# Performance work log

Measured on AMD Instinct MI355X. Metric: run time of the kernel, lower is better.

Reference implementation:

```python
import math
import jax, jax.numpy as jnp
import numpy as np

B, N, E, H, U = 8, 1024, 256, 4, 6
HD = E // H // 2  # head_dim = embed_dim // num_heads // 2 = 32
DEPTH = 1
LAMBDA_INIT = 1.0 - math.exp(-1.0 / DEPTH)


def setup_inputs() -> dict:
    key = jax.random.key(0)
    ks = jax.random.split(key, 8)
    x = jax.random.normal(ks[0], (B, N, E), dtype=jnp.float32)
    u = jax.random.normal(ks[1], (B, U, N, N), dtype=jnp.float32)
    # bool mask, True = masked out; p=0.2 so no row is fully masked
    umask = jax.random.bernoulli(ks[2], 0.2, (B, N, N, 1))
    v_w = jax.random.normal(ks[3], (E, E), dtype=jnp.float32) * (E ** -0.5)
    out_w = jax.random.normal(ks[4], (E, E), dtype=jnp.float32) * (E ** -0.5)
    u_w = jax.random.normal(ks[5], (2 * H, U), dtype=jnp.float32) * (U ** -0.5)  # 1x1 conv weight
    u_b = jnp.zeros((2 * H,), dtype=jnp.float32)
    lambda_q1 = jax.random.normal(ks[6], (100,), dtype=jnp.float32) * 0.1
    lambda_k1 = jax.random.normal(ks[7], (100,), dtype=jnp.float32) * 0.1
    return {"x": x, "u": u, "umask": umask, "v_w": v_w, "out_w": out_w,
            "u_w": u_w, "u_b": u_b, "lambda_q1": lambda_q1, "lambda_k1": lambda_k1}


def reference(x, u, umask, v_w, out_w, u_w, u_b, lambda_q1, lambda_k1):
    b, n, e = x.shape
    # v projection -> [B, H, N, 2*HD]
    v = jnp.einsum('bne,fe->bnf', x, v_w)
    v = v.reshape(b, n, H, 2 * HD).transpose(0, 2, 1, 3)
    # 1x1 conv over channel dim: [B, U, N, N] -> [B, 2H, N, N]
    scores = jnp.einsum('bcij,oc->boij', u, u_w) + u_b[None, :, None, None]
    # masked_fill with umask.transpose(3,1): [B,N,N,1] -> [B,1,N,N]
    mask = jnp.transpose(umask, (0, 3, 2, 1))
    scores = jnp.where(mask, -jnp.inf, scores)
    attn = jax.nn.softmax(scores, axis=-1)
    # differential beta (scalar)
    lambda_1 = jnp.exp(jnp.sum(lambda_q1 * lambda_k1))
    beta = jax.nn.sigmoid(lambda_1 * LAMBDA_INIT)
    attn = attn.reshape(b, H, 2, n, n)
    attn_w = attn[:, :, 0] - beta * attn[:, :, 1]  # [B, H, N, N]
    out = jnp.einsum('bhij,bhjd->bhid', attn_w, v)  # [B, H, N, 2HD]
    out = out.transpose(0, 2, 1, 3).reshape(b, n, e)
    out = jnp.einsum('bne,fe->bnf', out, out_w)
    return (out, attn_w, beta)
```

## Files before the change

### kernel.cpp

```cpp
#include <hip/hip_runtime.h>

#define Bb 8
#define Nn 1024
#define Ee 256
#define Hh 4
#define Uu 6
#define CH 8
#define HD2 64

static constexpr size_t OUT_ATTN = (size_t)Bb * Nn * Ee;
static constexpr size_t OUT_BETA = OUT_ATTN + (size_t)Bb * Hh * Nn * Nn;

static constexpr size_t WS_W     = 64;
static constexpr size_t WS_VT    = 512;
static constexpr size_t WS_MASKT = WS_VT + (size_t)Bb * Hh * HD2 * Nn * 2;
static constexpr size_t WS_OUTH  = WS_MASKT + (size_t)Bb * Nn * Nn;
static constexpr size_t WS_ATTNB = WS_OUTH + (size_t)Bb * Nn * Ee * 2;

typedef __attribute__((ext_vector_type(8))) short short8;
typedef __attribute__((ext_vector_type(4))) float floatx4;
typedef __attribute__((ext_vector_type(4))) unsigned short ushort4v;
typedef __attribute__((ext_vector_type(4))) unsigned char uchar4v;

__device__ __forceinline__ float bf2f(unsigned short h) {
  unsigned u = ((unsigned)h) << 16;
  return __builtin_bit_cast(float, u);
}
__device__ __forceinline__ unsigned short f2bf(float f) {
  unsigned u = __builtin_bit_cast(unsigned, f);
  u += 0x7FFFu + ((u >> 16) & 1u);
  return (unsigned short)(u >> 16);
}
__device__ __forceinline__ float ldf(const void* p, size_t i, int dtf) {
  return dtf ? ((const float*)p)[i] : bf2f(((const unsigned short*)p)[i]);
}
__device__ __forceinline__ short8 ld8(const void* p, size_t i, int dtf) {
  short8 r;
  if (dtf) {
    const float* f = (const float*)p + i;
    floatx4 a = *(const floatx4*)f;
    floatx4 b = *(const floatx4*)(f + 4);
    r[0]=(short)f2bf(a[0]); r[1]=(short)f2bf(a[1]); r[2]=(short)f2bf(a[2]); r[3]=(short)f2bf(a[3]);
    r[4]=(short)f2bf(b[0]); r[5]=(short)f2bf(b[1]); r[6]=(short)f2bf(b[2]); r[7]=(short)f2bf(b[3]);
  } else {
    r = *(const short8*)((const unsigned short*)p + i);
  }
  return r;
}
__device__ __forceinline__ floatx4 ld4(const void* p, size_t i, int dtf) {
  floatx4 r;
  if (dtf) {
    r = *(const floatx4*)((const float*)p + i);
  } else {
    ushort4v u = *(const ushort4v*)((const unsigned short*)p + i);
    r[0]=bf2f(u[0]); r[1]=bf2f(u[1]); r[2]=bf2f(u[2]); r[3]=bf2f(u[3]);
  }
  return r;
}
__device__ __forceinline__ float clampf(float v) {
  return fminf(fmaxf(v, -1e4f), 1e4f);
}

__global__ __launch_bounds__(128) void k0_init(
    const unsigned char* __restrict__ um,
    const void* __restrict__ xp,
    const void* __restrict__ uw,
    const void* __restrict__ ub,
    const void* __restrict__ lq,
    const void* __restrict__ lk,
    void* __restrict__ ws,
    float* __restrict__ out) {
  __shared__ int flags, cnt;
  __shared__ float ps[128];
  const int tid = threadIdx.x;
  if (tid == 0) { flags = 0; cnt = 0; }
  __syncthreads();
  int f = 0;
  for (int idx = tid; idx < 4096; idx += 128) {
    unsigned char bv = um[idx];
    int m4 = idx & 3;
    if (bv == 1 || bv == 0xFF) f |= (m4 == 0) ? 1 : 2;
    if (bv == 0x3F) { if (m4 == 3) f |= 8; else if (m4 == 1) f |= 16; }
  }
  atomicOr(&flags, f);
  unsigned wb = ((const unsigned*)xp)[tid];
  unsigned eL = (wb >> 7) & 0xFF;
  if (eL >= 100 && eL <= 135) atomicAdd(&cnt, 1);
  __syncthreads();
  const int dtf = (cnt < 64) ? 1 : 0;
  if (tid < 64) {
    int o = tid >> 3, c = tid & 7;
    float v = 0.f;
    if (c < 6)      v = clampf(ldf(uw, (size_t)o * Uu + c, dtf));
    else if (c == 6) v = clampf(ldf(ub, o, dtf));
    ((float*)ws)[16 + tid] = v;
  }
  float p = 0.f;
  if (tid < 100) p = ldf(lq, tid, dtf) * ldf(lk, tid, dtf);
  ps[tid] = p;
  __syncthreads();
  for (int s = 64; s > 0; s >>= 1) {
    if (tid < s) ps[tid] += ps[tid + s];
    __syncthreads();
  }
  if (tid == 0) {
    int fl = flags;
    int kind = (fl & 2) ? 1 : (fl & 1) ? 0 : (fl & 16) ? 2 : (fl & 8) ? 3 : 0;
    ((int*)ws)[1] = kind;
    ((int*)ws)[2] = dtf;
    float s0 = ps[0];
    if (!(s0 > -30.f && s0 < 30.f)) s0 = 0.f;
    float lambda1 = __expf(s0);
    float beta = 1.f / (1.f + __expf(-lambda1 * 0.63212055882855767840f));
    ((float*)ws)[0] = beta;
    out[OUT_BETA] = beta;
  }
}

__global__ __launch_bounds__(256) void k1_maskt(const void* __restrict__ um,
                                                void* __restrict__ ws) {
  const int kind = ((const int*)ws)[1];
  unsigned char* maskt = (unsigned char*)ws + WS_MASKT;
  __shared__ unsigned char tile[64][65];
  const int b = blockIdx.z, i0 = blockIdx.x * 64, j0 = blockIdx.y * 64;
  const int tid = threadIdx.x, tx = tid & 63, ty = tid >> 6;
#pragma unroll
  for (int p = 0; p < 16; ++p) {
    int jl = ty + 4 * p;
    size_t src = ((size_t)(b * Nn + j0 + jl)) * Nn + i0 + tx;
    unsigned char v;
    if (kind == 0)      v = (((const int*)um)[src] != 0);
    else if (kind == 1) v = (((const unsigned char*)um)[src] != 0);
    else if (kind == 2) v = (((const unsigned short*)um)[src] != 0);
    else                v = (((const float*)um)[src] != 0.f);
    tile[jl][tx] = v;
  }
  __syncthreads();
#pragma unroll
  for (int p = 0; p < 16; ++p) {
    int il = ty + 4 * p;
    maskt[((size_t)(b * Nn + i0 + il)) * Nn + j0 + tx] = tile[tx][il];
  }
}

__global__ __launch_bounds__(256) void k2_vproj(
    const void* __restrict__ x,
    const void* __restrict__ vw,
    void* __restrict__ ws) {
  const int dtf = ((const int*)ws)[2];
  const int bid = blockIdx.x;
  const int fb = bid & 3;
  const int base = (bid >> 2) * 64;
  const int tid = threadIdx.x;
  const int wave = tid >> 6, lane = tid & 63;
  const int q = lane >> 4, m = lane & 15;
  const int b = base >> 10;
  const int nloc = base & 1023;

  floatx4 acc[4] = {{0,0,0,0},{0,0,0,0},{0,0,0,0},{0,0,0,0}};
  const size_t arow = (size_t)(base + 16 * wave + m) * Ee;
#pragma unroll
  for (int k0 = 0; k0 < Ee; k0 += 32) {
    short8 a = ld8(x, arow + k0 + q * 8, dtf);
#pragma unroll
    for (int ct = 0; ct < 4; ++ct) {
      short8 bfr = ld8(vw, (size_t)(fb * 64 + ct * 16 + m) * Ee + k0 + q * 8, dtf);
      acc[ct] = __builtin_amdgcn_mfma_f32_16x16x32_bf16(a, bfr, acc[ct], 0, 0, 0);
    }
  }
  unsigned short* vt = (unsigned short*)((char*)ws + WS_VT);
#pragma unroll
  for (int ct = 0; ct < 4; ++ct) {
    int d = ct * 16 + m;
    int n0w = nloc + 16 * wave + q * 4;
    ushort4v vals;
#pragma unroll
    for (int t = 0; t < 4; ++t) vals[t] = f2bf(acc[ct][t]);
    *(ushort4v*)(vt + ((size_t)((b * Hh + fb) * HD2 + d)) * Nn + n0w) = vals;
  }
}

__global__ __launch_bounds__(256, 4) void k3_softmax(
    const void* __restrict__ u,
    void* __restrict__ ws,
    float* __restrict__ out) {
  const int dtf = ((const int*)ws)[2];
  const int tid = threadIdx.x;
  const int bid = blockIdx.x;
  const int b = bid >> 10;
  const int i = bid & 1023;
  const int lane = tid & 63;
  const int wave = tid >> 6;
  const int j0 = tid * 4;

  const float beta = ((const float*)ws)[0];
  const float* wsw = (const float*)ws + 16;
  const unsigned char* maskt = (const unsigned char*)ws + WS_MASKT;
  unsigned short* attnb = (unsigned short*)((char*)ws + WS_ATTNB);
  __shared__ float red[4][CH];

  float uc[Uu][4];
#pragma unroll
  for (int c = 0; c < Uu; ++c) {
    floatx4 uv = ld4(u, ((size_t)(b * Uu + c) * Nn + i) * Nn + j0, dtf);
#pragma unroll
    for (int jj = 0; jj < 4; ++jj) uc[c][jj] = clampf(uv[jj]);
  }
  uchar4v mk = *(const uchar4v*)(maskt + ((size_t)(b * Nn + i)) * Nn + j0);

  float w[CH][Uu], bo[CH];
#pragma unroll
  for (int o = 0; o < CH; ++o) {
    floatx4 a = *(const floatx4*)(wsw + o * 8);
    floatx4 c4 = *(const floatx4*)(wsw + o * 8 + 4);
    w[o][0]=a[0]; w[o][1]=a[1]; w[o][2]=a[2]; w[o][3]=a[3];
    w[o][4]=c4[0]; w[o][5]=c4[1]; bo[o]=c4[2];
  }

  float s[CH][4], sm[CH];
#pragma unroll
  for (int o = 0; o < CH; ++o) {
    float acc = 0.f;
#pragma unroll
    for (int jj = 0; jj < 4; ++jj) {
      float v = bo[o];
#pragma unroll
      for (int c = 0; c < Uu; ++c) v = fmaf(w[o][c], uc[c][jj], v);
      v = fminf(v, 30.f);
      if (mk[jj]) v = -1e30f;
      float e = __expf(v);
      s[o][jj] = e;
      acc += e;
    }
#pragma unroll
    for (int off = 32; off > 0; off >>= 1) acc += __shfl_xor(acc, off, 64);
    sm[o] = acc;
  }
  if (lane == 0) {
#pragma unroll
    for (int o = 0; o < CH; ++o) red[wave][o] = sm[o];
  }
  __syncthreads();
#pragma unroll
  for (int o = 0; o < CH; ++o)
    sm[o] = 1.f / (red[0][o] + red[1][o] + red[2][o] + red[3][o]);

#pragma unroll
  for (int h = 0; h < Hh; ++h) {
    floatx4 ov;
    ushort4v ob;
#pragma unroll
    for (int jj = 0; jj < 4; ++jj) {
      ov[jj] = s[2 * h][jj] * sm[2 * h] - beta * (s[2 * h + 1][jj] * sm[2 * h + 1]);
      ob[jj] = f2bf(ov[jj]);
    }
    const size_t off = ((size_t)((b * Hh + h) * Nn + i)) * Nn + j0;
    *(floatx4*)(out + OUT_ATTN + off) = ov;
    *(ushort4v*)(attnb + off) = ob;
  }
}

__global__ __launch_bounds__(256) void k4_pv(
    void* __restrict__ ws) {
  const int bid = blockIdx.x;
  const int it = bid & 31, h = (bid >> 5) & 3, b = bid >> 7;
  const int tid = threadIdx.x;
  const int wave = tid >> 6, lane = tid & 63;
  const int q = lane >> 4, m = lane & 15;
  const int rh = wave & 1, cp = wave >> 1;
  const int i0 = it * 32 + rh * 16;

  const unsigned short* attnb = (const unsigned short*)((const char*)ws + WS_ATTNB);
  const unsigned short* vt = (const unsigned short*)((const char*)ws + WS_VT);

  floatx4 acc[2] = {{0,0,0,0},{0,0,0,0}};
  const size_t abase = ((size_t)((b * Hh + h) * Nn + i0 + m)) * Nn;
  const size_t vtb = (size_t)(b * Hh + h) * HD2;
#pragma unroll 4
  for (int k0 = 0; k0 < Nn; k0 += 32) {
    short8 a = *(const short8*)(attnb + abase + k0 + q * 8);
#pragma unroll
    for (int c2 = 0; c2 < 2; ++c2) {
      int ct = cp * 2 + c2;
      short8 bfr = *(const short8*)(vt + (vtb + ct * 16 + m) * Nn + k0 + q * 8);
      acc[c2] = __builtin_amdgcn_mfma_f32_16x16x32_bf16(a, bfr, acc[c2], 0, 0, 0);
    }
  }
  unsigned short* outh = (unsigned short*)((char*)ws + WS_OUTH);
#pragma unroll
  for (int c2 = 0; c2 < 2; ++c2) {
    int ct = cp * 2 + c2;
#pragma unroll
    for (int t = 0; t < 4; ++t) {
      int irow = i0 + q * 4 + t;
      outh[((size_t)(b * Nn + irow)) * Ee + h * HD2 + ct * 16 + m] = f2bf(acc[c2][t]);
    }
  }
}

__global__ __launch_bounds__(256) void k5_oproj(
    const void* __restrict__ ow,
    const void* __restrict__ ws,
    float* __restrict__ out) {
  const int dtf = ((const int*)ws)[2];
  const int bid = blockIdx.x;
  const int fb = bid & 3;
  const int g = (bid >> 2) * 64;
  const int tid = threadIdx.x;
  const int wave = tid >> 6, lane = tid & 63;
  const int q = lane >> 4, m = lane & 15;

  const unsigned short* outh = (const unsigned short*)((const char*)ws + WS_OUTH);
  floatx4 acc[4] = {{0,0,0,0},{0,0,0,0},{0,0,0,0},{0,0,0,0}};
  const size_t awrow = (size_t)(fb * 64 + 16 * wave + m) * Ee;
#pragma unroll
  for (int k0 = 0; k0 < Ee; k0 += 32) {
    short8 a = ld8(ow, awrow + k0 + q * 8, dtf);
#pragma unroll
    for (int ct = 0; ct < 4; ++ct) {
      short8 bfr = *(const short8*)(outh + (size_t)(g + ct * 16 + m) * Ee + k0 + q * 8);
      acc[ct] = __builtin_amdgcn_mfma_f32_16x16x32_bf16(a, bfr, acc[ct], 0, 0, 0);
    }
  }
#pragma unroll
  for (int ct = 0; ct < 4; ++ct) {
    int nrow = g + ct * 16 + m;
    floatx4 vals;
#pragma unroll
    for (int t = 0; t < 4; ++t) vals[t] = acc[ct][t];
    *(floatx4*)(out + (size_t)nrow * Ee + fb * 64 + 16 * wave + q * 4) = vals;
  }
}

extern "C" void kernel_launch(void* const* d_in, const int* in_sizes, int n_in,
                              void* d_out, int out_size, void* d_ws, size_t ws_size,
                              hipStream_t stream) {
  (void)in_sizes; (void)n_in; (void)out_size; (void)ws_size;
  const void* x  = d_in[0];
  const void* u  = d_in[1];
  const void* umask = d_in[2];
  const void* vw = d_in[3];
  const void* ow = d_in[4];
  const void* uw = d_in[5];
  const void* ub = d_in[6];
  const void* lq = d_in[7];
  const void* lk = d_in[8];
  float* out = (float*)d_out;

  k0_init<<<1, 128, 0, stream>>>((const unsigned char*)umask, x, uw, ub, lq, lk, d_ws, out);
  k1_maskt<<<dim3(16, 16, 8), 256, 0, stream>>>(umask, d_ws);
  k2_vproj<<<512, 256, 0, stream>>>(x, vw, d_ws);
  k3_softmax<<<8192, 256, 0, stream>>>(u, d_ws, out);
  k4_pv<<<1024, 256, 0, stream>>>(d_ws);
  k5_oproj<<<512, 256, 0, stream>>>(ow, d_ws, out);
}
```

Measured before the change: 467.7 us.

## Drop init kernel, bit-pack transposed mask, recompute params per block

Removes the single-block init kernel. The dtype probe, mask-kind detection, conv weights and beta are now recomputed locally in each consuming kernel (ballot-based dtype probe, per-block weight table in shared memory). The transposed mask is stored as one bit per element instead of one byte, cutting the mask write and re-read traffic by about eight times. The softmax processes channels in two groups of four to lower register pressure, at the cost of an extra barrier and redundant per-block parameter loads.

New measurement: 466.1 us. No clear change (-0.3%).

```diff
diff --git a/kernel.cpp b/kernel.cpp
--- a/kernel.cpp
+++ b/kernel.cpp
@@ -11,16 +11,14 @@
 static constexpr size_t OUT_ATTN = (size_t)Bb * Nn * Ee;
 static constexpr size_t OUT_BETA = OUT_ATTN + (size_t)Bb * Hh * Nn * Nn;
 
-static constexpr size_t WS_W     = 64;
-static constexpr size_t WS_VT    = 512;
-static constexpr size_t WS_MASKT = WS_VT + (size_t)Bb * Hh * HD2 * Nn * 2;
-static constexpr size_t WS_OUTH  = WS_MASKT + (size_t)Bb * Nn * Nn;
+static constexpr size_t WS_VT    = 64;
+static constexpr size_t WS_MASKB = WS_VT + (size_t)Bb * Hh * HD2 * Nn * 2;
+static constexpr size_t WS_OUTH  = WS_MASKB + (size_t)Bb * Nn * (Nn / 8);
 static constexpr size_t WS_ATTNB = WS_OUTH + (size_t)Bb * Nn * Ee * 2;
 
 typedef __attribute__((ext_vector_type(8))) short short8;
 typedef __attribute__((ext_vector_type(4))) float floatx4;
 typedef __attribute__((ext_vector_type(4))) unsigned short ushort4v;
-typedef __attribute__((ext_vector_type(4))) unsigned char uchar4v;
 
 __device__ __forceinline__ float bf2f(unsigned short h) {
   unsigned u = ((unsigned)h) << 16;
@@ -60,70 +58,39 @@
 __device__ __forceinline__ float clampf(float v) {
   return fminf(fmaxf(v, -1e4f), 1e4f);
 }
-
-__global__ __launch_bounds__(128) void k0_init(
-    const unsigned char* __restrict__ um,
-    const void* __restrict__ xp,
-    const void* __restrict__ uw,
-    const void* __restrict__ ub,
-    const void* __restrict__ lq,
-    const void* __restrict__ lk,
-    void* __restrict__ ws,
-    float* __restrict__ out) {
-  __shared__ int flags, cnt;
-  __shared__ float ps[128];
-  const int tid = threadIdx.x;
-  if (tid == 0) { flags = 0; cnt = 0; }
+__device__ __forceinline__ int probe_dtf(const void* x) {
+  unsigned wb = ((const unsigned*)x)[threadIdx.x & 63];
+  unsigned eL = (wb >> 7) & 0xFF;
+  unsigned long long bal = __ballot(eL >= 100u && eL <= 135u);
+  return (__popcll(bal) < 32) ? 1 : 0;
+}
+
+__global__ __launch_bounds__(256) void k1_maskt(const void* __restrict__ um,
+                                                void* __restrict__ ws) {
+  __shared__ unsigned char tile[64][65];
+  __shared__ int flagsL;
+  const int tid = threadIdx.x;
+  if (tid == 0) flagsL = 0;
   __syncthreads();
+  const unsigned char* umb = (const unsigned char*)um;
   int f = 0;
-  for (int idx = tid; idx < 4096; idx += 128) {
-    unsigned char bv = um[idx];
+#pragma unroll
+  for (int k = 0; k < 16; ++k) {
+    int idx = tid * 16 + k;
+    unsigned char bv = umb[idx];
     int m4 = idx & 3;
     if (bv == 1 || bv == 0xFF) f |= (m4 == 0) ? 1 : 2;
     if (bv == 0x3F) { if (m4 == 3) f |= 8; else if (m4 == 1) f |= 16; }
   }
-  atomicOr(&flags, f);
-  unsigned wb = ((const unsigned*)xp)[tid];
-  unsigned eL = (wb >> 7) & 0xFF;
-  if (eL >= 100 && eL <= 135) atomicAdd(&cnt, 1);
+#pragma unroll
+  for (int off = 32; off > 0; off >>= 1) f |= __shfl_xor(f, off, 64);
+  if ((tid & 63) == 0) atomicOr(&flagsL, f);
   __syncthreads();
-  const int dtf = (cnt < 64) ? 1 : 0;
-  if (tid < 64) {
-    int o = tid >> 3, c = tid & 7;
-    float v = 0.f;
-    if (c < 6)      v = clampf(ldf(uw, (size_t)o * Uu + c, dtf));
-    else if (c == 6) v = clampf(ldf(ub, o, dtf));
-    ((float*)ws)[16 + tid] = v;
-  }
-  float p = 0.f;
-  if (tid < 100) p = ldf(lq, tid, dtf) * ldf(lk, tid, dtf);
-  ps[tid] = p;
-  __syncthreads();
-  for (int s = 64; s > 0; s >>= 1) {
-    if (tid < s) ps[tid] += ps[tid + s];
-    __syncthreads();
-  }
-  if (tid == 0) {
-    int fl = flags;
-    int kind = (fl & 2) ? 1 : (fl & 1) ? 0 : (fl & 16) ? 2 : (fl & 8) ? 3 : 0;
-    ((int*)ws)[1] = kind;
-    ((int*)ws)[2] = dtf;
-    float s0 = ps[0];
-    if (!(s0 > -30.f && s0 < 30.f)) s0 = 0.f;
-    float lambda1 = __expf(s0);
-    float beta = 1.f / (1.f + __expf(-lambda1 * 0.63212055882855767840f));
-    ((float*)ws)[0] = beta;
-    out[OUT_BETA] = beta;
-  }
-}
-
-__global__ __launch_bounds__(256) void k1_maskt(const void* __restrict__ um,
-                                                void* __restrict__ ws) {
-  const int kind = ((const int*)ws)[1];
-  unsigned char* maskt = (unsigned char*)ws + WS_MASKT;
-  __shared__ unsigned char tile[64][65];
+  const int fl = flagsL;
+  const int kind = (fl & 2) ? 1 : (fl & 1) ? 0 : (fl & 16) ? 2 : (fl & 8) ? 3 : 0;
+
   const int b = blockIdx.z, i0 = blockIdx.x * 64, j0 = blockIdx.y * 64;
-  const int tid = threadIdx.x, tx = tid & 63, ty = tid >> 6;
+  const int tx = tid & 63, ty = tid >> 6;
 #pragma unroll
   for (int p = 0; p < 16; ++p) {
     int jl = ty + 4 * p;
@@ -136,10 +103,16 @@
     tile[jl][tx] = v;
   }
   __syncthreads();
-#pragma unroll
-  for (int p = 0; p < 16; ++p) {
-    int il = ty + 4 * p;
-    maskt[((size_t)(b * Nn + i0 + il)) * Nn + j0 + tx] = tile[tx][il];
+  unsigned char* maskb = (unsigned char*)ws + WS_MASKB;
+  const int jb = (j0 >> 3);
+#pragma unroll
+  for (int half = 0; half < 2; ++half) {
+    int it = tid + half * 256;
+    int il = it & 63, g = it >> 6;
+    unsigned v = 0;
+#pragma unroll
+    for (int k = 0; k < 8; ++k) v |= (unsigned)(tile[8 * g + k][il] & 1u) << k;
+    maskb[((size_t)(b * Nn + i0 + il)) * (Nn / 8) + jb + g] = (unsigned char)v;
   }
 }
 
@@ -147,7 +120,7 @@
     const void* __restrict__ x,
     const void* __restrict__ vw,
     void* __restrict__ ws) {
-  const int dtf = ((const int*)ws)[2];
+  const int dtf = probe_dtf(x);
   const int bid = blockIdx.x;
   const int fb = bid & 3;
   const int base = (bid >> 2) * 64;
@@ -182,9 +155,13 @@
 
 __global__ __launch_bounds__(256, 4) void k3_softmax(
     const void* __restrict__ u,
+    const void* __restrict__ x,
+    const void* __restrict__ uw,
+    const void* __restrict__ ub,
+    const void* __restrict__ lq,
+    const void* __restrict__ lk,
     void* __restrict__ ws,
     float* __restrict__ out) {
-  const int dtf = ((const int*)ws)[2];
   const int tid = threadIdx.x;
   const int bid = blockIdx.x;
   const int b = bid >> 10;
@@ -193,11 +170,7 @@
   const int wave = tid >> 6;
   const int j0 = tid * 4;
 
-  const float beta = ((const float*)ws)[0];
-  const float* wsw = (const float*)ws + 16;
-  const unsigned char* maskt = (const unsigned char*)ws + WS_MASKT;
-  unsigned short* attnb = (unsigned short*)((char*)ws + WS_ATTNB);
-  __shared__ float red[4][CH];
+  const int dtf = probe_dtf(x);
 
   float uc[Uu][4];
 #pragma unroll
@@ -206,57 +179,91 @@
 #pragma unroll
     for (int jj = 0; jj < 4; ++jj) uc[c][jj] = clampf(uv[jj]);
   }
-  uchar4v mk = *(const uchar4v*)(maskt + ((size_t)(b * Nn + i)) * Nn + j0);
-
-  float w[CH][Uu], bo[CH];
-#pragma unroll
-  for (int o = 0; o < CH; ++o) {
-    floatx4 a = *(const floatx4*)(wsw + o * 8);
-    floatx4 c4 = *(const floatx4*)(wsw + o * 8 + 4);
-    w[o][0]=a[0]; w[o][1]=a[1]; w[o][2]=a[2]; w[o][3]=a[3];
-    w[o][4]=c4[0]; w[o][5]=c4[1]; bo[o]=c4[2];
-  }
-
-  float s[CH][4], sm[CH];
-#pragma unroll
-  for (int o = 0; o < CH; ++o) {
-    float acc = 0.f;
-#pragma unroll
-    for (int jj = 0; jj < 4; ++jj) {
-      float v = bo[o];
-#pragma unroll
-      for (int c = 0; c < Uu; ++c) v = fmaf(w[o][c], uc[c][jj], v);
-      v = fminf(v, 30.f);
-      if (mk[jj]) v = -1e30f;
-      float e = __expf(v);
-      s[o][jj] = e;
-      acc += e;
-    }
-#pragma unroll
-    for (int off = 32; off > 0; off >>= 1) acc += __shfl_xor(acc, off, 64);
-    sm[o] = acc;
-  }
-  if (lane == 0) {
-#pragma unroll
-    for (int o = 0; o < CH; ++o) red[wave][o] = sm[o];
+  const unsigned char* maskb = (const unsigned char*)ws + WS_MASKB;
+  const unsigned char mbyte = maskb[((size_t)(b * Nn + i)) * (Nn / 8) + (tid >> 1)];
+  const int msh = (tid & 1) * 4;
+
+  __shared__ float wtab[64];
+  __shared__ float betaL;
+  __shared__ float red[4][CH];
+  if (wave == 1) {
+    int o = lane >> 3, c = lane & 7;
+    float v = 0.f;
+    if (c < 6)      v = clampf(ldf(uw, (size_t)o * Uu + c, dtf));
+    else if (c == 6) v = clampf(ldf(ub, o, dtf));
+    wtab[lane] = v;
+  }
+  if (wave == 0) {
+    float p = ldf(lq, lane, dtf) * ldf(lk, lane, dtf);
+    if (lane < 36) p += ldf(lq, 64 + lane, dtf) * ldf(lk, 64 + lane, dtf);
+#pragma unroll
+    for (int off = 32; off > 0; off >>= 1) p += __shfl_xor(p, off, 64);
+    if (lane == 0) {
+      if (!(p > -30.f && p < 30.f)) p = 0.f;
+      float lambda1 = __expf(p);
+      float bta = 1.f / (1.f + __expf(-lambda1 * 0.63212055882855767840f));
+      betaL = bta;
+      if (bid == 0) out[OUT_BETA] = bta;
+    }
   }
   __syncthreads();
-#pragma unroll
-  for (int o = 0; o < CH; ++o)
-    sm[o] = 1.f / (red[0][o] + red[1][o] + red[2][o] + red[3][o]);
-
-#pragma unroll
-  for (int h = 0; h < Hh; ++h) {
-    floatx4 ov;
-    ushort4v ob;
-#pragma unroll
-    for (int jj = 0; jj < 4; ++jj) {
-      ov[jj] = s[2 * h][jj] * sm[2 * h] - beta * (s[2 * h + 1][jj] * sm[2 * h + 1]);
-      ob[jj] = f2bf(ov[jj]);
-    }
-    const size_t off = ((size_t)((b * Hh + h) * Nn + i)) * Nn + j0;
-    *(floatx4*)(out + OUT_ATTN + off) = ov;
-    *(ushort4v*)(attnb + off) = ob;
+  const float beta = betaL;
+  unsigned short* attnb = (unsigned short*)((char*)ws + WS_ATTNB);
+
+#pragma unroll
+  for (int g = 0; g < 2; ++g) {
+    float w[4][Uu], bo[4];
+#pragma unroll
+    for (int oo = 0; oo < 4; ++oo) {
+      const float* wr = wtab + (g * 4 + oo) * 8;
+#pragma unroll
+      for (int c = 0; c < Uu; ++c) w[oo][c] = wr[c];
+      bo[oo] = wr[6];
+    }
+    float s[4][4], sm[4];
+#pragma unroll
+    for (int oo = 0; oo < 4; ++oo) {
+      float acc = 0.f;
+#pragma unroll
+      for (int jj = 0; jj < 4; ++jj) {
+        float v = bo[oo];
+#pragma unroll
+        for (int c = 0; c < Uu; ++c) v = fmaf(w[oo][c], uc[c][jj], v);
+        v = fminf(v, 30.f);
+        if ((mbyte >> (msh + jj)) & 1) v = -1e30f;
+        float e = __expf(v);
+        s[oo][jj] = e;
+        acc += e;
+      }
+#pragma unroll
+      for (int off = 32; off > 0; off >>= 1) acc += __shfl_xor(acc, off, 64);
+      sm[oo] = acc;
+    }
+    if (lane == 0) {
+#pragma unroll
+      for (int oo = 0; oo < 4; ++oo) red[wave][g * 4 + oo] = sm[oo];
+    }
+    __syncthreads();
+#pragma unroll
+    for (int oo = 0; oo < 4; ++oo)
+      sm[oo] = 1.f / (red[0][g * 4 + oo] + red[1][g * 4 + oo] +
+                      red[2][g * 4 + oo] + red[3][g * 4 + oo]);
+
+#pragma unroll
+    for (int hh = 0; hh < 2; ++hh) {
+      int h = g * 2 + hh;
+      floatx4 ov;
+      ushort4v ob;
+#pragma unroll
+      for (int jj = 0; jj < 4; ++jj) {
+        float vv = s[2 * hh][jj] * sm[2 * hh] - beta * (s[2 * hh + 1][jj] * sm[2 * hh + 1]);
+        ov[jj] = vv;
+        ob[jj] = f2bf(vv);
+      }
+      const size_t off = ((size_t)((b * Hh + h) * Nn + i)) * Nn + j0;
+      *(floatx4*)(out + OUT_ATTN + off) = ov;
+      *(ushort4v*)(attnb + off) = ob;
+    }
   }
 }
 
@@ -300,9 +307,10 @@
 
 __global__ __launch_bounds__(256) void k5_oproj(
     const void* __restrict__ ow,
+    const void* __restrict__ x,
     const void* __restrict__ ws,
     float* __restrict__ out) {
-  const int dtf = ((const int*)ws)[2];
+  const int dtf = probe_dtf(x);
   const int bid = blockIdx.x;
   const int fb = bid & 3;
   const int g = (bid >> 2) * 64;
@@ -347,10 +355,9 @@
   const void* lk = d_in[8];
   float* out = (float*)d_out;
 
-  k0_init<<<1, 128, 0, stream>>>((const unsigned char*)umask, x, uw, ub, lq, lk, d_ws, out);
   k1_maskt<<<dim3(16, 16, 8), 256, 0, stream>>>(umask, d_ws);
   k2_vproj<<<512, 256, 0, stream>>>(x, vw, d_ws);
-  k3_softmax<<<8192, 256, 0, stream>>>(u, d_ws, out);
+  k3_softmax<<<8192, 256, 0, stream>>>(u, x, uw, ub, lq, lk, d_ws, out);
   k4_pv<<<1024, 256, 0, stream>>>(d_ws);
-  k5_oproj<<<512, 256, 0, stream>>>(ow, d_ws, out);
-}
+  k5_oproj<<<512, 256, 0, stream>>>(ow, x, d_ws, out);
+}
```
